# Optimization experiments

Measured on AMD Instinct MI355X. Metric: run time of the kernel, lower is better.

## Reference

```python
import jax, jax.numpy as jnp
import numpy as np
from jax import lax

DN = ('NHWC', 'HWIO', 'NHWC')
N_MEM = 2000  # memory slots
BN_EPS = 1e-3


def _conv(x, w, b):
    # tf.nn.conv2d stride 2, SAME, NHWC / HWIO
    return lax.conv_general_dilated(x, w, (2, 2), 'SAME', dimension_numbers=DN) + b


def _convt(x, w, b):
    # tf.nn.conv2d_transpose; w is TF layout [kh, kw, out_ch, in_ch]
    return lax.conv_transpose(x, w, (2, 2), 'SAME', dimension_numbers=DN,
                              transpose_kernel=True) + b


def _bn(x, g, b):
    # BatchNormalization(training=True): batch statistics over N,H,W
    m = jnp.mean(x, axis=(0, 1, 2))
    v = jnp.var(x, axis=(0, 1, 2))
    return g * (x - m) * lax.rsqrt(v + BN_EPS) + b


def setup_inputs() -> dict:
    key = jax.random.key(0)
    ks = iter(jax.random.split(key, 40))
    def gn(shape, s=0.05):
        return jax.random.normal(next(ks), shape, jnp.float32) * s
    inp = {'x': jax.random.uniform(next(ks), (16, 256, 256, 3), jnp.float32)}
    inp.update(
        w_e1=gn((1, 1, 3, 16)), b_e1=gn((16,)),
        g_bn1=jnp.ones(16, jnp.float32), be_bn1=jnp.zeros(16, jnp.float32),
        w_e2=gn((3, 3, 16, 32)), b_e2=gn((32,)),
        g_bn2=jnp.ones(32, jnp.float32), be_bn2=jnp.zeros(32, jnp.float32),
        w_e3=gn((3, 3, 32, 64)), b_e3=gn((64,)),
        g_bn3=jnp.ones(64, jnp.float32), be_bn3=jnp.zeros(64, jnp.float32),
        w_mem=gn((1, 1, N_MEM, 64)),
        w_d1=gn((3, 3, 32, 64)), b_d1=gn((32,)),
        g_bnt1=jnp.ones(32, jnp.float32), be_bnt1=jnp.zeros(32, jnp.float32),
        w_d2=gn((3, 3, 16, 32)), b_d2=gn((16,)),
        g_bnt2=jnp.ones(16, jnp.float32), be_bnt2=jnp.zeros(16, jnp.float32),
        w_d3=gn((3, 3, 3, 16)), b_d3=gn((3,)),
    )
    return inp


def reference(x, w_e1, b_e1, g_bn1, be_bn1, w_e2, b_e2, g_bn2, be_bn2,
              w_e3, b_e3, g_bn3, be_bn3, w_mem,
              w_d1, b_d1, g_bnt1, be_bnt1, w_d2, b_d2, g_bnt2, be_bnt2,
              w_d3, b_d3):
    # ---- encode ----
    h = jax.nn.relu(_bn(_conv(x, w_e1, b_e1), g_bn1, be_bn1))   # [B,128,128,16]
    h = jax.nn.relu(_bn(_conv(h, w_e2, b_e2), g_bn2, be_bn2))   # [B,64,64,32]
    z = jax.nn.relu(_bn(_conv(h, w_e3, b_e3), g_bn3, be_bn3))   # [B,32,32,64]
    # ---- memory addressing ----
    mem = w_mem[0, 0]                                            # [N, 64]
    num = jnp.einsum('bhwc,nc->bhwn', z, mem)
    den = jnp.einsum('bhwc,nc->bhwn', z * z, mem * mem)
    att = jax.nn.softmax((num + 1e-12) / (den + 1e-12), axis=-1)  # [B,32,32,N]
    d = att - 1.0 / N_MEM                                        # hard shrinkage
    renorm = jnp.clip(jax.nn.relu(d) * att / (jnp.abs(d) + 1e-12),
                      1e-12, 1.0 - 1e-12)
    z_hat = jnp.einsum('bhwn,nc->bhwc', renorm, mem)             # [B,32,32,64]
    # ---- decode ----
    t = jax.nn.relu(_bn(_convt(z_hat, w_d1, b_d1), g_bnt1, be_bnt1))  # [B,64,64,32]
    t = jax.nn.relu(_bn(_convt(t, w_d2, b_d2), g_bnt2, be_bnt2))      # [B,128,128,16]
    x_hat = jnp.clip(_convt(t, w_d3, b_d3), 1e-12, 1.0 - 1e-12)       # [B,256,256,3]
    return x_hat
```

## Files before the change

### kernel.cpp

```cpp
#include <hip/hip_runtime.h>
#include <math.h>

typedef __bf16 bf16x8 __attribute__((ext_vector_type(8)));
typedef __bf16 bf16x4 __attribute__((ext_vector_type(4)));
typedef float  f32x16 __attribute__((ext_vector_type(16)));

static __device__ __forceinline__ f32x16 zero16() {
  f32x16 v;
  #pragma unroll
  for (int i = 0; i < 16; ++i) v[i] = 0.f;
  return v;
}
static __device__ __forceinline__ unsigned int bfbits(__bf16 b) {
  return (unsigned int)__builtin_bit_cast(unsigned short, b);
}
static __device__ __forceinline__ bf16x8 mk8(unsigned int a, unsigned int b,
                                             unsigned int c, unsigned int d) {
  uint4 t; t.x = a; t.y = b; t.z = c; t.w = d;
  return __builtin_bit_cast(bf16x8, t);
}

__global__ __launch_bounds__(256) void k_conv1(const float* __restrict__ x,
    const float* __restrict__ w, const float* __restrict__ b, float* __restrict__ y,
    float* __restrict__ partials) {
  int t = blockIdx.x*256 + threadIdx.x;
  int ox = t & 127, oy = (t >> 7) & 127, bb = t >> 14;
  const float* xp = x + ((size_t)((bb*256 + 2*oy)*256 + 2*ox))*3;
  float x0 = xp[0], x1 = xp[1], x2 = xp[2];
  float4 rg[4];
  float4* yp = (float4*)(y + (size_t)t*16);
  #pragma unroll
  for (int g = 0; g < 4; ++g) {
    float4 r;
    r.x = b[g*4+0] + x0*w[g*4+0] + x1*w[16+g*4+0] + x2*w[32+g*4+0];
    r.y = b[g*4+1] + x0*w[g*4+1] + x1*w[16+g*4+1] + x2*w[32+g*4+1];
    r.z = b[g*4+2] + x0*w[g*4+2] + x1*w[16+g*4+2] + x2*w[32+g*4+2];
    r.w = b[g*4+3] + x0*w[g*4+3] + x1*w[16+g*4+3] + x2*w[32+g*4+3];
    rg[g] = r;
    yp[g] = r;
  }
  float4 s4[4], q4[4];
  #pragma unroll
  for (int g=0; g<4; ++g) {
    s4[g] = rg[g];
    q4[g] = make_float4(rg[g].x*rg[g].x, rg[g].y*rg[g].y, rg[g].z*rg[g].z, rg[g].w*rg[g].w);
  }
  #pragma unroll
  for (int off=1; off<64; off<<=1) {
    #pragma unroll
    for (int g=0; g<4; ++g) {
      s4[g].x += __shfl_xor(s4[g].x, off); s4[g].y += __shfl_xor(s4[g].y, off);
      s4[g].z += __shfl_xor(s4[g].z, off); s4[g].w += __shfl_xor(s4[g].w, off);
      q4[g].x += __shfl_xor(q4[g].x, off); q4[g].y += __shfl_xor(q4[g].y, off);
      q4[g].z += __shfl_xor(q4[g].z, off); q4[g].w += __shfl_xor(q4[g].w, off);
    }
  }
  __shared__ float red[4][32];
  int wv = threadIdx.x >> 6, lane = threadIdx.x & 63;
  if (lane == 0) {
    #pragma unroll
    for (int g=0; g<4; ++g) {
      *(float4*)&red[wv][g*4]      = s4[g];
      *(float4*)&red[wv][16 + g*4] = q4[g];
    }
  }
  __syncthreads();
  if (threadIdx.x < 32)
    partials[(size_t)blockIdx.x*32 + threadIdx.x] =
      red[0][threadIdx.x]+red[1][threadIdx.x]+red[2][threadIdx.x]+red[3][threadIdx.x];
}

template<int C,int CSPLIT>
__global__ __launch_bounds__(256) void k_finalize2(const float* __restrict__ partials, int nblk,
    double inv_n, const float* __restrict__ g, const float* __restrict__ be, float* __restrict__ ss) {
  const int COUTT = C/CSPLIT;
  const int NSTAT = 2*C;
  const int PER = 256/NSTAT;
  __shared__ double red[256];
  int tid = threadIdx.x;
  int st = tid % NSTAT, sub = tid / NSTAT;
  int c = st % C, kind = st / C;
  int cq = c / COUTT, j = c % COUTT;
  int nb = nblk / CSPLIT;
  double acc = 0.0;
  #pragma unroll 4
  for (int i = sub; i < nb; i += PER) {
    int bq = cq + i*CSPLIT;
    acc += (double)partials[(size_t)bq*2*COUTT + kind*COUTT + j];
  }
  red[tid] = acc;
  __syncthreads();
  for (int off = PER>>1; off > 0; off >>= 1) {
    if (sub < off) red[tid] += red[tid + off*NSTAT];
    __syncthreads();
  }
  if (tid < C) {
    double mean = red[tid]*inv_n;
    double var  = red[C+tid]*inv_n - mean*mean;
    float scale = g[tid] * rsqrtf((float)var + 1e-3f);
    float shift = be[tid] - (float)mean*scale;
    ss[tid] = scale; ss[C+tid] = shift;
  }
}

template<int CIN,int COUT,int CSPLIT,int HIN,int HOUT,bool BN>
__global__ __launch_bounds__(256) void k_conv_bn(const float* __restrict__ in,
    const float* __restrict__ w, const float* __restrict__ bias,
    const float* __restrict__ ss, float* __restrict__ y, float* __restrict__ partials) {
  const int COUTT = COUT/CSPLIT;
  const int NW4 = COUTT/4;
  __shared__ float4 wlds[9*CIN*NW4];
  int bid = blockIdx.x;
  int cq  = bid % CSPLIT;
  int pxb = bid / CSPLIT;
  int c0  = cq*COUTT;
  for (int e = threadIdx.x; e < 9*CIN*NW4; e += 256) {
    int r = e / NW4, cg = e % NW4;
    wlds[e] = *(const float4*)(w + (size_t)r*COUT + c0 + cg*4);
  }
  __syncthreads();
  int t0 = pxb*256 + threadIdx.x;
  float4 acc[NW4];
  #pragma unroll
  for (int g=0; g<NW4; ++g) acc[g] = *(const float4*)(bias + c0 + g*4);
  int ox = t0 % HOUT, oy = (t0/HOUT) % HOUT, bb = t0/(HOUT*HOUT);
  #pragma unroll 1
  for (int dy=0; dy<3; ++dy) {
    #pragma unroll 1
    for (int dx=0; dx<3; ++dx) {
      int tap = dy*3+dx;
      int iy = 2*oy + dy, ix = 2*ox + dx;
      if (iy < HIN && ix < HIN) {
        const float* bp = in + ((size_t)(bb*HIN + iy)*HIN + ix)*CIN;
        #pragma unroll
        for (int ci4=0; ci4<CIN/4; ++ci4) {
          float4 v = *(const float4*)(bp + ci4*4);
          if (BN) {
            float4 sc = *(const float4*)(ss + ci4*4);
            float4 sh = *(const float4*)(ss + CIN + ci4*4);
            v.x = fmaxf(0.f, fmaf(v.x, sc.x, sh.x));
            v.y = fmaxf(0.f, fmaf(v.y, sc.y, sh.y));
            v.z = fmaxf(0.f, fmaf(v.z, sc.z, sh.z));
            v.w = fmaxf(0.f, fmaf(v.w, sc.w, sh.w));
          }
          float va[4] = {v.x, v.y, v.z, v.w};
          #pragma unroll
          for (int k=0;k<4;++k) {
            float vk = va[k];
            #pragma unroll
            for (int g=0; g<NW4; ++g) {
              float4 w4 = wlds[(tap*CIN + ci4*4 + k)*NW4 + g];
              acc[g].x = fmaf(vk, w4.x, acc[g].x);
              acc[g].y = fmaf(vk, w4.y, acc[g].y);
              acc[g].z = fmaf(vk, w4.z, acc[g].z);
              acc[g].w = fmaf(vk, w4.w, acc[g].w);
            }
          }
        }
      }
    }
  }
  float4* yp = (float4*)(y + (size_t)t0*COUT + c0);
  #pragma unroll
  for (int g=0;g<NW4;++g) yp[g] = acc[g];
  float4 s4[NW4], q4[NW4];
  #pragma unroll
  for (int g=0; g<NW4; ++g) {
    s4[g] = acc[g];
    q4[g] = make_float4(acc[g].x*acc[g].x, acc[g].y*acc[g].y,
                        acc[g].z*acc[g].z, acc[g].w*acc[g].w);
  }
  #pragma unroll
  for (int off=1; off<64; off<<=1) {
    #pragma unroll
    for (int g=0; g<NW4; ++g) {
      s4[g].x += __shfl_xor(s4[g].x, off); s4[g].y += __shfl_xor(s4[g].y, off);
      s4[g].z += __shfl_xor(s4[g].z, off); s4[g].w += __shfl_xor(s4[g].w, off);
      q4[g].x += __shfl_xor(q4[g].x, off); q4[g].y += __shfl_xor(q4[g].y, off);
      q4[g].z += __shfl_xor(q4[g].z, off); q4[g].w += __shfl_xor(q4[g].w, off);
    }
  }
  __shared__ float red[4][2*COUTT];
  int wv = threadIdx.x >> 6, lane = threadIdx.x & 63;
  if (lane == 0) {
    #pragma unroll
    for (int g=0; g<NW4; ++g) {
      *(float4*)&red[wv][g*4]         = s4[g];
      *(float4*)&red[wv][COUTT + g*4] = q4[g];
    }
  }
  __syncthreads();
  if (threadIdx.x < 2*COUTT)
    partials[(size_t)bid*2*COUTT + threadIdx.x] =
      red[0][threadIdx.x]+red[1][threadIdx.x]+red[2][threadIdx.x]+red[3][threadIdx.x];
}


__global__ __launch_bounds__(256) void k_prep_z(const float* __restrict__ y3,
    const float* __restrict__ ss,
    __bf16* __restrict__ ZH, __bf16* __restrict__ ZL,
    __bf16* __restrict__ Z2H, __bf16* __restrict__ Z2L) {
  int t = blockIdx.x*256 + threadIdx.x;
  float4 v = ((const float4*)y3)[t];
  int c0 = (t*4) & 63;
  float4 sc = *(const float4*)(ss + c0);
  float4 sh = *(const float4*)(ss + 64 + c0);
  float vv[4];
  vv[0] = fmaxf(0.f, fmaf(v.x, sc.x, sh.x));
  vv[1] = fmaxf(0.f, fmaf(v.y, sc.y, sh.y));
  vv[2] = fmaxf(0.f, fmaf(v.z, sc.z, sh.z));
  vv[3] = fmaxf(0.f, fmaf(v.w, sc.w, sh.w));
  bf16x4 h, l, h2, l2;
  #pragma unroll
  for (int i=0;i<4;++i) {
    float f = vv[i];
    __bf16 hb = (__bf16)f;
    h[i] = hb; l[i] = (__bf16)(f - (float)hb);
    float q = f*f;
    __bf16 qb = (__bf16)q;
    h2[i] = qb; l2[i] = (__bf16)(q - (float)qb);
  }
  ((bf16x4*)ZH)[t] = h;  ((bf16x4*)ZL)[t] = l;
  ((bf16x4*)Z2H)[t] = h2; ((bf16x4*)Z2L)[t] = l2;
}

__global__ __launch_bounds__(256) void k_prep_m(const float* __restrict__ mem,
    __bf16* __restrict__ MH, __bf16* __restrict__ ML,
    __bf16* __restrict__ M2H, __bf16* __restrict__ M2L,
    __bf16* __restrict__ MHT, __bf16* __restrict__ MLT) {
  int t = blockIdx.x*256 + threadIdx.x;
  int n = t >> 4, c0 = (t & 15)*4;
  float4 v = make_float4(0.f,0.f,0.f,0.f);
  if (n < 2000) v = *(const float4*)(mem + (size_t)n*64 + c0);
  float vv[4] = {v.x, v.y, v.z, v.w};
  bf16x4 h, l, h2, l2;
  #pragma unroll
  for (int i=0;i<4;++i) {
    float f = vv[i];
    __bf16 hb = (__bf16)f;
    h[i] = hb; l[i] = (__bf16)(f - (float)hb);
    float q = f*f;
    __bf16 qb = (__bf16)q;
    h2[i] = qb; l2[i] = (__bf16)(q - (float)qb);
  }
  *(bf16x4*)(MH  + (size_t)n*64 + c0) = h;
  *(bf16x4*)(ML  + (size_t)n*64 + c0) = l;
  *(bf16x4*)(M2H + (size_t)n*64 + c0) = h2;
  *(bf16x4*)(M2L + (size_t)n*64 + c0) = l2;
  #pragma unroll
  for (int i=0;i<4;++i) {
    MHT[(size_t)(c0+i)*2048 + n] = h[i];
    MLT[(size_t)(c0+i)*2048 + n] = l[i];
  }
}

__global__ __launch_bounds__(256) void k_pass1(
    const __bf16* __restrict__ ZH, const __bf16* __restrict__ ZL,
    const __bf16* __restrict__ Z2H, const __bf16* __restrict__ Z2L,
    const __bf16* __restrict__ MH, const __bf16* __restrict__ ML,
    const __bf16* __restrict__ M2H, const __bf16* __restrict__ M2L,
    __bf16* __restrict__ U, float* __restrict__ MT,
    float* __restrict__ partM, float* __restrict__ partS) {
  int chunk = blockIdx.x & 15, pbg = blockIdx.x >> 4;
  int wave = threadIdx.x >> 6, lane = threadIdx.x & 63;
  int p0 = pbg*128 + wave*32;
  int col = lane & 31, hi = lane >> 5;
  bf16x8 bzh[4], bzl[4], b2h[4], b2l[4];
  size_t zoff = (size_t)(p0 + col)*64 + hi*8;
  #pragma unroll
  for (int ks=0;ks<4;++ks) {
    bzh[ks] = *(const bf16x8*)(ZH  + zoff + ks*16);
    bzl[ks] = *(const bf16x8*)(ZL  + zoff + ks*16);
    b2h[ks] = *(const bf16x8*)(Z2H + zoff + ks*16);
    b2l[ks] = *(const bf16x8*)(Z2L + zoff + ks*16);
  }
  float tmaxv[4], ssumv[4];
  int nbase = chunk*128;
  #pragma unroll
  for (int t=0; t<4; ++t) {
    int n0 = nbase + t*32;
    size_t arow = (size_t)(n0 + col)*64 + hi*8;
    f32x16 num = zero16(), den = zero16();
    #pragma unroll
    for (int ks=0;ks<4;++ks) {
      bf16x8 amh = *(const bf16x8*)(MH + arow + ks*16);
      bf16x8 aml = *(const bf16x8*)(ML + arow + ks*16);
      num = __builtin_amdgcn_mfma_f32_32x32x16_bf16(amh, bzh[ks], num, 0,0,0);
      num = __builtin_amdgcn_mfma_f32_32x32x16_bf16(amh, bzl[ks], num, 0,0,0);
      num = __builtin_amdgcn_mfma_f32_32x32x16_bf16(aml, bzh[ks], num, 0,0,0);
      bf16x8 a2h = *(const bf16x8*)(M2H + arow + ks*16);
      bf16x8 a2l = *(const bf16x8*)(M2L + arow + ks*16);
      den = __builtin_amdgcn_mfma_f32_32x32x16_bf16(a2h, b2h[ks], den, 0,0,0);
      den = __builtin_amdgcn_mfma_f32_32x32x16_bf16(a2h, b2l[ks], den, 0,0,0);
      den = __builtin_amdgcn_mfma_f32_32x32x16_bf16(a2l, b2h[ks], den, 0,0,0);
    }
    bool maskt = (n0 + 32 > 2000);
    float sv[16];
    float tmax = -3.4e38f;
    #pragma unroll
    for (int r=0;r<16;++r) {
      float s = (num[r] + 1e-12f) * __builtin_amdgcn_rcpf(den[r] + 1e-12f);
      if (maskt) {
        int nn = n0 + (r&3) + 8*(r>>2) + 4*hi;
        if (nn >= 2000) s = -3.4e38f;
      }
      sv[r] = s;
      tmax = fmaxf(tmax, s);
    }
    float ssum = 0.f;
    unsigned int up[8];
    #pragma unroll
    for (int j=0;j<8;++j) {
      float u0 = __expf(sv[2*j]   - tmax);
      float u1 = __expf(sv[2*j+1] - tmax);
      ssum += u0; ssum += u1;
      up[j] = bfbits((__bf16)u0) | (bfbits((__bf16)u1) << 16);
    }
    size_t idx = (size_t)((chunk*4 + t)*16384 + p0 + col)*2 + hi;
    uint4 st0; st0.x = up[0]; st0.y = up[1]; st0.z = up[2]; st0.w = up[3];
    uint4 st1; st1.x = up[4]; st1.y = up[5]; st1.z = up[6]; st1.w = up[7];
    *(uint4*)(U + idx*16)     = st0;
    *(uint4*)(U + idx*16 + 8) = st1;
    MT[idx] = tmax;
    tmaxv[t] = tmax; ssumv[t] = ssum;
  }
  float m = fmaxf(fmaxf(tmaxv[0], tmaxv[1]), fmaxf(tmaxv[2], tmaxv[3]));
  float S = ssumv[0]*__expf(tmaxv[0]-m) + ssumv[1]*__expf(tmaxv[1]-m)
          + ssumv[2]*__expf(tmaxv[2]-m) + ssumv[3]*__expf(tmaxv[3]-m);
  float mo = __shfl_xor(m, 32);
  float So = __shfl_xor(S, 32);
  float mf = fmaxf(m, mo);
  float Sf = S*__expf(m - mf) + So*__expf(mo - mf);
  if (lane < 32) {
    int p = p0 + col;
    partM[chunk*16384 + p] = mf;
    partS[chunk*16384 + p] = Sf;
  }
}

__global__ __launch_bounds__(256) void k_pass2(
    const __bf16* __restrict__ U, const float* __restrict__ MT,
    const __bf16* __restrict__ MHT, const __bf16* __restrict__ MLT,
    const float* __restrict__ partM, const float* __restrict__ partS,
    __bf16* __restrict__ ZPb) {
  int chunk = blockIdx.x & 7, pbg = blockIdx.x >> 3;
  int wave = threadIdx.x >> 6, lane = threadIdx.x & 63;
  int p0 = pbg*128 + wave*32;
  int col = lane & 31, hi = lane >> 5;
  int p = p0 + col;
  float pmv[16];
  float Mp = -3.4e38f;
  #pragma unroll
  for (int c=0;c<16;++c) { pmv[c] = partM[c*16384 + p]; Mp = fmaxf(Mp, pmv[c]); }
  float Ssum = 0.f;
  #pragma unroll
  for (int c=0;c<16;++c) Ssum += partS[c*16384 + p] * __expf(pmv[c] - Mp);
  float CM  = Mp + __logf(Ssum);
  float thr = CM - 7.6009025f;
  f32x16 za0 = zero16(), za1 = zero16();
  int nbase = chunk*256;
  #pragma unroll 2
  for (int t=0; t<8; ++t) {
    int n0 = nbase + t*32;
    size_t idx = (size_t)((chunk*8 + t)*16384 + p)*2 + hi;
    uint4 a = *(const uint4*)(U + idx*16);
    uint4 b = *(const uint4*)(U + idx*16 + 8);
    float mt = MT[idx];
    float scale = __expf(mt - CM);
    float thru  = __expf(thr - mt);
    unsigned int ua[8] = {a.x,a.y,a.z,a.w,b.x,b.y,b.z,b.w};
    unsigned int qh[8];
    #pragma unroll
    for (int j=0;j<8;++j) {
      float u0 = __builtin_bit_cast(float, ua[j] << 16);
      float u1 = __builtin_bit_cast(float, ua[j] & 0xffff0000u);
      float r0 = (u0 > thru) ? u0*scale : 0.f;
      float r1 = (u1 > thru) ? u1*scale : 0.f;
      qh[j] = bfbits((__bf16)r0) | (bfbits((__bf16)r1) << 16);
    }
    unsigned int qhp[8];
    #pragma unroll
    for (int i=0;i<8;++i) qhp[i] = (unsigned int)__shfl_xor((int)qh[i], 32);
    bf16x8 f1h = hi ? mk8(qhp[2],qhp[3],qh[2],qh[3]) : mk8(qh[0],qh[1],qhp[0],qhp[1]);
    bf16x8 f2h = hi ? mk8(qhp[6],qhp[7],qh[6],qh[7]) : mk8(qh[4],qh[5],qhp[4],qhp[5]);
    #pragma unroll
    for (int kh=0; kh<2; ++kh) {
      bf16x8 fh = kh ? f2h : f1h;
      size_t bofs = (size_t)col*2048 + n0 + kh*16 + hi*8;
      bf16x8 bmh0 = *(const bf16x8*)(MHT + bofs);
      bf16x8 bml0 = *(const bf16x8*)(MLT + bofs);
      bf16x8 bmh1 = *(const bf16x8*)(MHT + bofs + (size_t)32*2048);
      bf16x8 bml1 = *(const bf16x8*)(MLT + bofs + (size_t)32*2048);
      za0 = __builtin_amdgcn_mfma_f32_32x32x16_bf16(fh, bmh0, za0, 0,0,0);
      za0 = __builtin_amdgcn_mfma_f32_32x32x16_bf16(fh, bml0, za0, 0,0,0);
      za1 = __builtin_amdgcn_mfma_f32_32x32x16_bf16(fh, bmh1, za1, 0,0,0);
      za1 = __builtin_amdgcn_mfma_f32_32x32x16_bf16(fh, bml1, za1, 0,0,0);
    }
  }
  size_t base = (size_t)chunk << 20;
  #pragma unroll
  for (int r=0;r<16;++r) {
    int prow = (r&3) + 8*(r>>2) + 4*hi;
    size_t o = base + (size_t)(p0 + prow)*64 + col;
    ZPb[o]      = (__bf16)za0[r];
    ZPb[o + 32] = (__bf16)za1[r];
  }
}

__global__ __launch_bounds__(256) void k_zcomb(const __bf16* __restrict__ ZPb,
                                               float* __restrict__ Gz) {
  int t = blockIdx.x*256 + threadIdx.x;
  float a = 0.f;
  #pragma unroll
  for (int c=0;c<8;++c) a += (float)ZPb[(size_t)c*1048576 + t];
  Gz[t] = a;
}

template<int CIN,int COUT,int CSPLIT,int HIN,bool BN>
__global__ __launch_bounds__(256) void k_convt_bn(const float* __restrict__ in,
    const float* __restrict__ w, const float* __restrict__ bias,
    const float* __restrict__ ss, float* __restrict__ y, float* __restrict__ partials) {
  const int COUTT = COUT/CSPLIT;
  const int HOUT = 2*HIN;
  __shared__ float4 wlds[4*COUTT*(CIN/4)];
  int bid = blockIdx.x;
  int cq = bid % CSPLIT; int rest = bid / CSPLIT;
  int cls = rest % 4;    int pxb = rest / 4;
  int pm = cls >> 1, pn = cls & 1;
  int c0 = cq*COUTT;
  int NTI = (pm == 0) ? 2 : 1;
  int NTJ = (pn == 0) ? 2 : 1;
  int NT = NTI*NTJ;
  for (int e = threadIdx.x; e < NT*COUTT*(CIN/4); e += 256) {
    int tl = e / (COUTT*(CIN/4));
    int rem = e % (COUTT*(CIN/4));
    int cc = rem / (CIN/4), ci4 = rem % (CIN/4);
    int ki = pm + 2*(tl / NTJ), kj = pn + 2*(tl % NTJ);
    wlds[e] = *(const float4*)(w + ((size_t)(ki*3+kj)*COUT + c0 + cc)*CIN + ci4*4);
  }
  __syncthreads();
  int t0 = pxb*256 + threadIdx.x;
  float acc[COUTT];
  #pragma unroll
  for (int cc=0;cc<COUTT;++cc) acc[cc] = bias[c0+cc];
  int nx = t0 % HIN, my = (t0/HIN) % HIN, bb = t0/(HIN*HIN);
  #pragma unroll 1
  for (int ti=0; ti<NTI; ++ti) {
    #pragma unroll 1
    for (int tj=0; tj<NTJ; ++tj) {
      int tl = ti*NTJ + tj;
      int i = my - ti, j = nx - tj;
      if (i >= 0 && j >= 0) {
        const float* bp = in + ((size_t)(bb*HIN + i)*HIN + j)*CIN;
        #pragma unroll
        for (int ci4=0; ci4<CIN/4; ++ci4) {
          float4 v = *(const float4*)(bp + ci4*4);
          if (BN) {
            float4 sc = *(const float4*)(ss + ci4*4);
            float4 sh = *(const float4*)(ss + CIN + ci4*4);
            v.x = fmaxf(0.f, fmaf(v.x, sc.x, sh.x));
            v.y = fmaxf(0.f, fmaf(v.y, sc.y, sh.y));
            v.z = fmaxf(0.f, fmaf(v.z, sc.z, sh.z));
            v.w = fmaxf(0.f, fmaf(v.w, sc.w, sh.w));
          }
          #pragma unroll
          for (int cc=0;cc<COUTT;++cc) {
            float4 w4 = wlds[(tl*COUTT + cc)*(CIN/4) + ci4];
            float a = acc[cc];
            a = fmaf(v.x, w4.x, a);
            a = fmaf(v.y, w4.y, a);
            a = fmaf(v.z, w4.z, a);
            a = fmaf(v.w, w4.w, a);
            acc[cc] = a;
          }
        }
      }
    }
  }
  int m = 2*my + pm, n = 2*nx + pn;
  float* yp = y + ((size_t)(bb*HOUT + m)*HOUT + n)*COUT + c0;
  #pragma unroll
  for (int g=0;g<COUTT/4;++g)
    ((float4*)yp)[g] = make_float4(acc[g*4], acc[g*4+1], acc[g*4+2], acc[g*4+3]);
  float s[COUTT], q[COUTT];
  #pragma unroll
  for (int cc=0;cc<COUTT;++cc) { s[cc] = acc[cc]; q[cc] = acc[cc]*acc[cc]; }
  #pragma unroll
  for (int off=1; off<64; off<<=1) {
    #pragma unroll
    for (int cc=0;cc<COUTT;++cc) {
      s[cc] += __shfl_xor(s[cc], off);
      q[cc] += __shfl_xor(q[cc], off);
    }
  }
  __shared__ float red[4][2*COUTT];
  int wv = threadIdx.x >> 6, lane = threadIdx.x & 63;
  if (lane == 0) {
    #pragma unroll
    for (int cc=0;cc<COUTT;++cc) { red[wv][cc] = s[cc]; red[wv][COUTT+cc] = q[cc]; }
  }
  __syncthreads();
  if (threadIdx.x < 2*COUTT)
    partials[(size_t)bid*2*COUTT + threadIdx.x] =
      red[0][threadIdx.x]+red[1][threadIdx.x]+red[2][threadIdx.x]+red[3][threadIdx.x];
}

__global__ __launch_bounds__(256) void k_convt_final(const float* __restrict__ in,
    const float* __restrict__ w, const float* __restrict__ bias,
    const float* __restrict__ ss, float* __restrict__ out) {
  const int CIN=16, HIN=128, HOUT=256;
  __shared__ float4 wlds[4*3*4];
  int cls = blockIdx.x & 3;
  int pxb = blockIdx.x >> 2;
  int pm = cls >> 1, pn = cls & 1;
  int NTI = (pm == 0) ? 2 : 1;
  int NTJ = (pn == 0) ? 2 : 1;
  int NT = NTI*NTJ;
  if (threadIdx.x < NT*3*4) {
    int e = threadIdx.x;
    int tl = e / 12, rem = e % 12;
    int c = rem / 4, ci4 = rem % 4;
    int ki = pm + 2*(tl / NTJ), kj = pn + 2*(tl % NTJ);
    wlds[e] = *(const float4*)(w + ((size_t)(ki*3+kj)*3 + c)*CIN + ci4*4);
  }
  __syncthreads();
  int t = pxb*256 + threadIdx.x;
  int nx = t % HIN, my = (t/HIN) % HIN, bb = t/(HIN*HIN);
  float a0 = bias[0], a1 = bias[1], a2 = bias[2];
  #pragma unroll 1
  for (int ti=0; ti<NTI; ++ti) {
    #pragma unroll 1
    for (int tj=0; tj<NTJ; ++tj) {
      int tl = ti*NTJ + tj;
      int i = my - ti, j = nx - tj;
      if (i >= 0 && j >= 0) {
        const float* bp = in + ((size_t)(bb*HIN + i)*HIN + j)*CIN;
        #pragma unroll
        for (int ci4=0; ci4<4; ++ci4) {
          float4 v = *(const float4*)(bp + ci4*4);
          float4 sc = *(const float4*)(ss + ci4*4);
          float4 sh = *(const float4*)(ss + CIN + ci4*4);
          v.x = fmaxf(0.f, fmaf(v.x, sc.x, sh.x));
          v.y = fmaxf(0.f, fmaf(v.y, sc.y, sh.y));
          v.z = fmaxf(0.f, fmaf(v.z, sc.z, sh.z));
          v.w = fmaxf(0.f, fmaf(v.w, sc.w, sh.w));
          float4 w0 = wlds[(tl*3 + 0)*4 + ci4];
          float4 w1 = wlds[(tl*3 + 1)*4 + ci4];
          float4 w2 = wlds[(tl*3 + 2)*4 + ci4];
          a0 = fmaf(v.x, w0.x, a0); a0 = fmaf(v.y, w0.y, a0);
          a0 = fmaf(v.z, w0.z, a0); a0 = fmaf(v.w, w0.w, a0);
          a1 = fmaf(v.x, w1.x, a1); a1 = fmaf(v.y, w1.y, a1);
          a1 = fmaf(v.z, w1.z, a1); a1 = fmaf(v.w, w1.w, a1);
          a2 = fmaf(v.x, w2.x, a2); a2 = fmaf(v.y, w2.y, a2);
          a2 = fmaf(v.z, w2.z, a2); a2 = fmaf(v.w, w2.w, a2);
        }
      }
    }
  }
  int m = 2*my + pm, n = 2*nx + pn;
  float* op = out + ((size_t)(bb*HOUT + m)*HOUT + n)*3;
  op[0] = fminf(fmaxf(a0, 1e-12f), 1.0f);
  op[1] = fminf(fmaxf(a1, 1e-12f), 1.0f);
  op[2] = fminf(fmaxf(a2, 1e-12f), 1.0f);
}

extern "C" void kernel_launch(void* const* d_in, const int* in_sizes, int n_in,
                              void* d_out, int out_size, void* d_ws, size_t ws_size,
                              hipStream_t stream) {
  const float* x    = (const float*)d_in[0];
  const float* w_e1 = (const float*)d_in[1];
  const float* b_e1 = (const float*)d_in[2];
  const float* g1   = (const float*)d_in[3];
  const float* be1  = (const float*)d_in[4];
  const float* w_e2 = (const float*)d_in[5];
  const float* b_e2 = (const float*)d_in[6];
  const float* g2   = (const float*)d_in[7];
  const float* be2  = (const float*)d_in[8];
  const float* w_e3 = (const float*)d_in[9];
  const float* b_e3 = (const float*)d_in[10];
  const float* g3   = (const float*)d_in[11];
  const float* be3  = (const float*)d_in[12];
  const float* wmem = (const float*)d_in[13];
  const float* w_d1 = (const float*)d_in[14];
  const float* b_d1 = (const float*)d_in[15];
  const float* gt1  = (const float*)d_in[16];
  const float* bet1 = (const float*)d_in[17];
  const float* w_d2 = (const float*)d_in[18];
  const float* b_d2 = (const float*)d_in[19];
  const float* gt2  = (const float*)d_in[20];
  const float* bet2 = (const float*)d_in[21];
  const float* w_d3 = (const float*)d_in[22];
  const float* b_d3 = (const float*)d_in[23];
  float* out = (float*)d_out;

  float* ws = (float*)d_ws;
  __bf16* U  = (__bf16*)ws;
  float* A   = ws;
  float* Cc  = ws + 4194304;
  float* Gz  = ws + 16777216;
  __bf16* ZPb = (__bf16*)(Gz + 1048576);
  float* E   = Gz + 1048576 + 8388608;
  float* bfbase = E + 1048576;
  __bf16* ZH  = (__bf16*)bfbase;
  __bf16* ZL  = ZH  + 16384*64;
  __bf16* Z2H = ZL  + 16384*64;
  __bf16* Z2L = Z2H + 16384*64;
  __bf16* MH  = Z2L + 16384*64;
  __bf16* ML  = MH  + 2048*64;
  __bf16* M2H = ML  + 2048*64;
  __bf16* M2L = M2H + 2048*64;
  __bf16* MHT = M2L + 2048*64;
  __bf16* MLT = MHT + 64*2048;
  float* PT   = (float*)(MLT + 64*2048);
  float* SS   = PT + 131072;
  float* PM   = SS + 256;
  float* PS   = PM + 262144;
  float* MT   = PS + 262144;
  (void)ws_size; (void)in_sizes; (void)n_in; (void)out_size;

  k_conv1<<<1024,256,0,stream>>>(x, w_e1, b_e1, A, PT);
  k_finalize2<16,1><<<1,256,0,stream>>>(PT, 1024, 1.0/262144.0, g1, be1, SS);
  k_conv_bn<16,32,2,128,64,true><<<512,256,0,stream>>>(A, w_e2, b_e2, SS, Cc, PT);
  k_finalize2<32,2><<<1,256,0,stream>>>(PT, 512, 1.0/65536.0, g2, be2, SS);
  k_conv_bn<32,64,8,64,32,true><<<512,256,0,stream>>>(Cc, w_e3, b_e3, SS, E, PT);
  k_finalize2<64,8><<<1,256,0,stream>>>(PT, 512, 1.0/16384.0, g3, be3, SS);
  k_prep_m<<<128,256,0,stream>>>(wmem, MH, ML, M2H, M2L, MHT, MLT);
  k_prep_z<<<1024,256,0,stream>>>(E, SS, ZH, ZL, Z2H, Z2L);
  k_pass1<<<2048,256,0,stream>>>(ZH, ZL, Z2H, Z2L, MH, ML, M2H, M2L, U, MT, PM, PS);
  k_pass2<<<1024,256,0,stream>>>(U, MT, MHT, MLT, PM, PS, ZPb);
  k_zcomb<<<4096,256,0,stream>>>(ZPb, Gz);
  k_convt_bn<64,32,2,32,false><<<512,256,0,stream>>>(Gz, w_d1, b_d1, nullptr, Cc, PT);
  k_finalize2<32,2><<<1,256,0,stream>>>(PT, 512, 1.0/65536.0, gt1, bet1, SS);
  k_convt_bn<32,16,1,64,true><<<1024,256,0,stream>>>(Cc, w_d2, b_d2, SS, A, PT);
  k_finalize2<16,1><<<1,256,0,stream>>>(PT, 1024, 1.0/262144.0, gt2, bet2, SS);
  k_convt_final<<<4096,256,0,stream>>>(A, w_d3, b_d3, SS, out);
}
```

Baseline: 357.7 us.

## Fuse z_hat chunk reduction into pass2 via LDS and drop low-part memory MFMAs

pass2 now gives each block 32 pixels, with the four waves splitting the 2000 memory slots. The per-wave partial z_hat tiles are summed in shared memory and written directly as fp32 Gz. This removes the bf16 partial buffer and the separate k_zcomb kernel. It also drops the low-order bf16 correction term of the memory matrix (MLT), halving the MFMAs and B loads in pass2 at the cost of some precision in z_hat. Grid size halves to 512 blocks, which lowers parallelism.

```diff
diff --git a/kernel.cpp b/kernel.cpp
--- a/kernel.cpp
+++ b/kernel.cpp
@@ -227,7 +227,7 @@
 __global__ __launch_bounds__(256) void k_prep_m(const float* __restrict__ mem,
     __bf16* __restrict__ MH, __bf16* __restrict__ ML,
     __bf16* __restrict__ M2H, __bf16* __restrict__ M2L,
-    __bf16* __restrict__ MHT, __bf16* __restrict__ MLT) {
+    __bf16* __restrict__ MHT) {
   int t = blockIdx.x*256 + threadIdx.x;
   int n = t >> 4, c0 = (t & 15)*4;
   float4 v = make_float4(0.f,0.f,0.f,0.f);
@@ -250,7 +250,6 @@
   #pragma unroll
   for (int i=0;i<4;++i) {
     MHT[(size_t)(c0+i)*2048 + n] = h[i];
-    MLT[(size_t)(c0+i)*2048 + n] = l[i];
   }
 }
 
@@ -340,12 +339,13 @@
 
 __global__ __launch_bounds__(256) void k_pass2(
     const __bf16* __restrict__ U, const float* __restrict__ MT,
-    const __bf16* __restrict__ MHT, const __bf16* __restrict__ MLT,
+    const __bf16* __restrict__ MHT,
     const float* __restrict__ partM, const float* __restrict__ partS,
-    __bf16* __restrict__ ZPb) {
-  int chunk = blockIdx.x & 7, pbg = blockIdx.x >> 3;
+    float* __restrict__ Gz) {
+  __shared__ float zl[4][32][68];
+  int pbg = blockIdx.x;
   int wave = threadIdx.x >> 6, lane = threadIdx.x & 63;
-  int p0 = pbg*128 + wave*32;
+  int p0 = pbg*32;
   int col = lane & 31, hi = lane >> 5;
   int p = p0 + col;
   float pmv[16];
@@ -358,11 +358,11 @@
   float CM  = Mp + __logf(Ssum);
   float thr = CM - 7.6009025f;
   f32x16 za0 = zero16(), za1 = zero16();
-  int nbase = chunk*256;
   #pragma unroll 2
-  for (int t=0; t<8; ++t) {
-    int n0 = nbase + t*32;
-    size_t idx = (size_t)((chunk*8 + t)*16384 + p)*2 + hi;
+  for (int t=0; t<16; ++t) {
+    int tg = wave*16 + t;
+    int n0 = tg*32;
+    size_t idx = (size_t)(tg*16384 + p)*2 + hi;
     uint4 a = *(const uint4*)(U + idx*16);
     uint4 b = *(const uint4*)(U + idx*16 + 8);
     float mt = MT[idx];
@@ -388,32 +388,32 @@
       bf16x8 fh = kh ? f2h : f1h;
       size_t bofs = (size_t)col*2048 + n0 + kh*16 + hi*8;
       bf16x8 bmh0 = *(const bf16x8*)(MHT + bofs);
-      bf16x8 bml0 = *(const bf16x8*)(MLT + bofs);
       bf16x8 bmh1 = *(const bf16x8*)(MHT + bofs + (size_t)32*2048);
-      bf16x8 bml1 = *(const bf16x8*)(MLT + bofs + (size_t)32*2048);
       za0 = __builtin_amdgcn_mfma_f32_32x32x16_bf16(fh, bmh0, za0, 0,0,0);
-      za0 = __builtin_amdgcn_mfma_f32_32x32x16_bf16(fh, bml0, za0, 0,0,0);
       za1 = __builtin_amdgcn_mfma_f32_32x32x16_bf16(fh, bmh1, za1, 0,0,0);
-      za1 = __builtin_amdgcn_mfma_f32_32x32x16_bf16(fh, bml1, za1, 0,0,0);
-    }
-  }
-  size_t base = (size_t)chunk << 20;
+    }
+  }
   #pragma unroll
   for (int r=0;r<16;++r) {
     int prow = (r&3) + 8*(r>>2) + 4*hi;
-    size_t o = base + (size_t)(p0 + prow)*64 + col;
-    ZPb[o]      = (__bf16)za0[r];
-    ZPb[o + 32] = (__bf16)za1[r];
-  }
-}
-
-__global__ __launch_bounds__(256) void k_zcomb(const __bf16* __restrict__ ZPb,
-                                               float* __restrict__ Gz) {
-  int t = blockIdx.x*256 + threadIdx.x;
-  float a = 0.f;
-  #pragma unroll
-  for (int c=0;c<8;++c) a += (float)ZPb[(size_t)c*1048576 + t];
-  Gz[t] = a;
+    zl[wave][prow][col]      = za0[r];
+    zl[wave][prow][col + 32] = za1[r];
+  }
+  __syncthreads();
+  int tp = threadIdx.x >> 3;
+  int tc = (threadIdx.x & 7) * 8;
+  float4 s0 = make_float4(0.f,0.f,0.f,0.f);
+  float4 s1 = make_float4(0.f,0.f,0.f,0.f);
+  #pragma unroll
+  for (int w2=0; w2<4; ++w2) {
+    float4 a0 = *(const float4*)&zl[w2][tp][tc];
+    float4 a1 = *(const float4*)&zl[w2][tp][tc+4];
+    s0.x += a0.x; s0.y += a0.y; s0.z += a0.z; s0.w += a0.w;
+    s1.x += a1.x; s1.y += a1.y; s1.z += a1.z; s1.w += a1.w;
+  }
+  float* gp = Gz + (size_t)(p0 + tp)*64 + tc;
+  *(float4*)gp       = s0;
+  *(float4*)(gp + 4) = s1;
 }
 
 template<int CIN,int COUT,int CSPLIT,int HIN,bool BN>
@@ -598,7 +598,6 @@
   float* A   = ws;
   float* Cc  = ws + 4194304;
   float* Gz  = ws + 16777216;
-  __bf16* ZPb = (__bf16*)(Gz + 1048576);
   float* E   = Gz + 1048576 + 8388608;
   float* bfbase = E + 1048576;
   __bf16* ZH  = (__bf16*)bfbase;
@@ -624,11 +623,10 @@
   k_finalize2<32,2><<<1,256,0,stream>>>(PT, 512, 1.0/65536.0, g2, be2, SS);
   k_conv_bn<32,64,8,64,32,true><<<512,256,0,stream>>>(Cc, w_e3, b_e3, SS, E, PT);
   k_finalize2<64,8><<<1,256,0,stream>>>(PT, 512, 1.0/16384.0, g3, be3, SS);
-  k_prep_m<<<128,256,0,stream>>>(wmem, MH, ML, M2H, M2L, MHT, MLT);
+  k_prep_m<<<128,256,0,stream>>>(wmem, MH, ML, M2H, M2L, MHT);
   k_prep_z<<<1024,256,0,stream>>>(E, SS, ZH, ZL, Z2H, Z2L);
   k_pass1<<<2048,256,0,stream>>>(ZH, ZL, Z2H, Z2L, MH, ML, M2H, M2L, U, MT, PM, PS);
-  k_pass2<<<1024,256,0,stream>>>(U, MT, MHT, MLT, PM, PS, ZPb);
-  k_zcomb<<<4096,256,0,stream>>>(ZPb, Gz);
+  k_pass2<<<512,256,0,stream>>>(U, MT, MHT, PM, PS, Gz);
   k_convt_bn<64,32,2,32,false><<<512,256,0,stream>>>(Gz, w_d1, b_d1, nullptr, Cc, PT);
   k_finalize2<32,2><<<1,256,0,stream>>>(PT, 512, 1.0/65536.0, gt1, bet1, SS);
   k_convt_bn<32,16,1,64,true><<<1024,256,0,stream>>>(Cc, w_d2, b_d2, SS, A, PT);
```

Measured after the change: 340.4 us. -4.8%, faster.
